# Optimization experiments

Measured on AMD Instinct MI355X. Metric: run time of the kernel, lower is better.

## Reference

```python
import jax, jax.numpy as jnp
import numpy as np

N = 50000        # nodes
E = 1600000      # edges (before self loops)
IN = 128         # in_channels
HID = 32         # hidden_channels
HEADS = 4
OUT = 16         # out_channels
B = 512          # graphs in batch
NEG_SLOPE = 0.2  # PyG GATConv default


def _uniform(key, shape, fan_in):
    s = 1.0 / np.sqrt(fan_in)
    return jax.random.uniform(key, shape, jnp.float32, -s, s)


def setup_inputs() -> dict:
    key = jax.random.key(0)
    ks = jax.random.split(key, 12)
    x = jax.random.normal(ks[0], (N, IN), jnp.float32)
    edge_index = jax.random.randint(ks[1], (2, E), 0, N, dtype=jnp.int64)
    batch = jnp.sort(jax.random.randint(ks[2], (N,), 0, B, dtype=jnp.int64))
    return {
        "x": x,
        "edge_index": edge_index,
        "batch": batch,
        "W1": _uniform(ks[3], (IN, HEADS * HID), IN),
        "att_src": _uniform(ks[4], (HEADS, HID), HID),
        "att_dst": _uniform(ks[5], (HEADS, HID), HID),
        "b1": jnp.zeros((HEADS * HID,), jnp.float32),
        "lin1_w": _uniform(ks[6], (HEADS * HID, HID), HEADS * HID),
        "lin1_b": _uniform(ks[7], (HID,), HEADS * HID),
        "lin2_w": _uniform(ks[8], (HID, OUT), HID),
        "lin2_b": _uniform(ks[9], (OUT,), HID),
    }


def _gat_conv(x, src, dst, W1, att_src, att_dst, b1):
    # h: [N, H, C]
    h = (x @ W1).reshape(N, HEADS, HID)
    a_s = (h * att_src).sum(-1)   # [N, H]
    a_d = (h * att_dst).sum(-1)   # [N, H]
    # per-edge attention logits [E', H]
    alpha = jax.nn.leaky_relu(a_s[src] + a_d[dst], negative_slope=NEG_SLOPE)
    # segment softmax over incoming edges of each destination node
    amax = jax.lax.stop_gradient(jax.ops.segment_max(alpha, dst, num_segments=N))
    ex = jnp.exp(alpha - amax[dst])
    den = jax.ops.segment_sum(ex, dst, num_segments=N)
    a = ex / (den[dst] + 1e-16)
    # weighted scatter-aggregate of source features: [N, H, C]
    out = jax.ops.segment_sum(h[src] * a[:, :, None], dst, num_segments=N)
    return out.reshape(N, HEADS * HID) + b1


def reference(x, edge_index, batch, W1, att_src, att_dst, b1, lin1_w, lin1_b, lin2_w, lin2_b):
    # add self loops (PyG GATConv default add_self_loops=True)
    loop = jnp.arange(N, dtype=edge_index.dtype)
    src = jnp.concatenate([edge_index[0], loop])
    dst = jnp.concatenate([edge_index[1], loop])
    # dropout layers are identity in eval mode
    xh = jax.nn.elu(_gat_conv(x, src, dst, W1, att_src, att_dst, b1))
    g = jax.ops.segment_sum(xh, batch, num_segments=B)  # global_add_pool -> [B, H*C]
    g = g @ lin1_w + lin1_b
    return g @ lin2_w + lin2_b
```

## Files before the change

### kernel.cpp

```cpp
#include <hip/hip_runtime.h>
#include <hip/hip_bf16.h>
#include <hip/hip_fp16.h>

#define N_NODES 50000
#define E_EDGES 1600000
#define IN_CH 128
#define HID 32
#define HEADS 4
#define HC (HEADS * HID)
#define OUT_CH 16
#define B_GRAPHS 512
#define NEG_SLOPE 0.2f
#define CAP 96
#define NB 256
#define BNODES 196
#define PCAP 7168
#define ACHUNK 4096
#define APART 391
#define ROWS_PB 64
#define GEMM_BLOCKS 782

__device__ __forceinline__ unsigned short f2bf(float f) {
    unsigned int u = __float_as_uint(f);
    unsigned int r = (u + 0x7FFFu + ((u >> 16) & 1u)) >> 16;
    return (unsigned short)r;
}

__device__ __forceinline__ float lrelu_exp(float v) {
    v = v > 0.f ? v : NEG_SLOPE * v;
    return __expf(v);
}

__global__ __launch_bounds__(256) void k_fused(const float* __restrict__ x,
                                               const float* __restrict__ W1,
                                               const float* __restrict__ att_src,
                                               const float* __restrict__ att_dst,
                                               const int* __restrict__ ei,
                                               unsigned short* __restrict__ hb,
                                               float* __restrict__ a_s,
                                               float* __restrict__ a_d,
                                               int* __restrict__ gcur,
                                               unsigned int* __restrict__ ebuf,
                                               float* __restrict__ g) {
    __shared__ float smem[12288];
    const int t = threadIdx.x;

    if (blockIdx.x < APART) {
        int* scnt = (int*)smem;
        int* sbase = scnt + NB;
        const int e0 = blockIdx.x * ACHUNK;
        int e1 = e0 + ACHUNK; if (e1 > E_EDGES) e1 = E_EDGES;
        for (int i = t; i < NB; i += 256) scnt[i] = 0;
        __syncthreads();
        const int* __restrict__ dstp = ei + E_EDGES;
        for (int e = e0 + t; e < e1; e += 256) {
            int d = dstp[e];
            atomicAdd(&scnt[d / BNODES], 1);
        }
        __syncthreads();
        for (int b = t; b < NB; b += 256) {
            sbase[b] = atomicAdd(&gcur[b], scnt[b]);
            scnt[b] = 0;
        }
        __syncthreads();
        for (int e = e0 + t; e < e1; e += 256) {
            int d = dstp[e];
            int s = ei[e];
            int b = d / BNODES;
            int dl = d - b * BNODES;
            int pos = sbase[b] + atomicAdd(&scnt[b], 1);
            if (pos < PCAP)
                ebuf[(size_t)b * PCAP + pos] = ((unsigned int)dl << 16) | (unsigned int)s;
        }
        return;
    }

    float* sX = smem;
    float* sW = smem + 8192;
    const int bid = blockIdx.x - APART;
    const int n0 = bid * ROWS_PB;

    int gt = bid * 256 + t;
    if (gt < B_GRAPHS * HC) g[gt] = 0.f;

    for (int i = t; i < ROWS_PB * 32; i += 256) {
        int r = i >> 5, c4 = i & 31;
        int n = n0 + r;
        float4 v = (n < N_NODES) ? ((const float4*)x)[(size_t)n * 32 + c4]
                                 : make_float4(0.f, 0.f, 0.f, 0.f);
        ((float4*)sX)[i] = v;
    }

    float acc[8][4];
#pragma unroll
    for (int j = 0; j < 8; j++)
#pragma unroll
        for (int c = 0; c < 4; c++) acc[j][c] = 0.f;

    const int tx = t & 31;
    const int ty = t >> 5;

    for (int kb = 0; kb < 4; kb++) {
        __syncthreads();
        for (int i = t; i < 32 * 32; i += 256) {
            ((float4*)sW)[i] =
                ((const float4*)W1)[(size_t)(kb * 32 + (i >> 5)) * 32 + (i & 31)];
        }
        __syncthreads();
#pragma unroll
        for (int kk = 0; kk < 32; kk += 4) {
            float4 w0 = *(float4*)&sW[(kk + 0) * 128 + tx * 4];
            float4 w1 = *(float4*)&sW[(kk + 1) * 128 + tx * 4];
            float4 w2 = *(float4*)&sW[(kk + 2) * 128 + tx * 4];
            float4 w3 = *(float4*)&sW[(kk + 3) * 128 + tx * 4];
#pragma unroll
            for (int j = 0; j < 8; j++) {
                float4 xv = *(float4*)&sX[(ty * 8 + j) * 128 + kb * 32 + kk];
                acc[j][0] += xv.x * w0.x + xv.y * w1.x + xv.z * w2.x + xv.w * w3.x;
                acc[j][1] += xv.x * w0.y + xv.y * w1.y + xv.z * w2.y + xv.w * w3.y;
                acc[j][2] += xv.x * w0.z + xv.y * w1.z + xv.z * w2.z + xv.w * w3.z;
                acc[j][3] += xv.x * w0.w + xv.y * w1.w + xv.z * w2.w + xv.w * w3.w;
            }
        }
    }

#pragma unroll
    for (int j = 0; j < 8; j++) {
        int n = n0 + ty * 8 + j;
        if (n < N_NODES) {
            ushort4 o;
            o.x = f2bf(acc[j][0]); o.y = f2bf(acc[j][1]);
            o.z = f2bf(acc[j][2]); o.w = f2bf(acc[j][3]);
            *(ushort4*)&hb[(size_t)n * HC + tx * 4] = o;
        }
    }

    __syncthreads();
    float* sH = smem;
#pragma unroll
    for (int j = 0; j < 8; j++) {
        float* row = &sH[(ty * 8 + j) * 129 + tx * 4];
        row[0] = acc[j][0]; row[1] = acc[j][1];
        row[2] = acc[j][2]; row[3] = acc[j][3];
    }
    __syncthreads();
    if (t < 128) {
        int r = t & 63;
        int n = n0 + r;
        const float* __restrict__ av = (t < 64) ? att_src : att_dst;
        float s0 = 0.f, s1 = 0.f, s2 = 0.f, s3 = 0.f;
#pragma unroll 4
        for (int j = 0; j < 32; j++) {
            const float* row = &sH[r * 129 + j];
            s0 += row[0]  * av[j];
            s1 += row[32] * av[32 + j];
            s2 += row[64] * av[64 + j];
            s3 += row[96] * av[96 + j];
        }
        if (n < N_NODES) {
            float* dst = (t < 64) ? a_s : a_d;
            *(float4*)(dst + (size_t)n * 4) = make_float4(s0, s1, s2, s3);
        }
    }
}

__global__ __launch_bounds__(256) void k_partB(const unsigned int* __restrict__ ebuf,
                                               const int* __restrict__ gcur,
                                               unsigned short* __restrict__ csr,
                                               int* __restrict__ cnt) {
    __shared__ unsigned short sbuf[BNODES * CAP];
    __shared__ int scnt[BNODES];
    const int t = threadIdx.x;
    const int b = blockIdx.x;
    const int dbase = b * BNODES;
    for (int i = t; i < BNODES; i += 256) {
        int d = dbase + i;
        scnt[i] = (d < N_NODES) ? 1 : 0;
        sbuf[i * CAP] = (unsigned short)d;
    }
    __syncthreads();
    int m = gcur[b]; if (m > PCAP) m = PCAP;
    for (int i = t; i < m; i += 256) {
        unsigned int p = ebuf[(size_t)b * PCAP + i];
        int dl = p >> 16;
        int s = p & 0xFFFFu;
        int c = atomicAdd(&scnt[dl], 1);
        if (c < CAP) sbuf[dl * CAP + c] = (unsigned short)s;
    }
    __syncthreads();
    const uint4* sb4 = (const uint4*)sbuf;
    uint4* g4 = (uint4*)(csr + (size_t)dbase * CAP);
    for (int i = t; i < (BNODES * CAP * 2) / 16; i += 256) g4[i] = sb4[i];
    for (int i = t; i < BNODES; i += 256) cnt[dbase + i] = scnt[i];
}

#define ANW 4
__global__ __launch_bounds__(256) void k_agg_pool(const int* __restrict__ cnt,
                                                  const unsigned short* __restrict__ csr,
                                                  const float* __restrict__ a_s,
                                                  const float* __restrict__ a_d,
                                                  const unsigned short* __restrict__ hb,
                                                  const float* __restrict__ b1,
                                                  const int* __restrict__ batch,
                                                  float* __restrict__ g) {
    __shared__ int   sS[4][CAP];
    __shared__ float sWt[4][4][100];
    const int t = threadIdx.x;
    const int wv = t >> 6;
    const int l = t & 63;
    const int head = l >> 4;
    const int c0 = 2 * l;
    const int n0 = blockIdx.x * (4 * ANW) + wv * ANW;
    const float2 bias = *(const float2*)(b1 + c0);
    float pool0 = 0.f, pool1 = 0.f;
    int cur = batch[n0];
    for (int n = n0; n < n0 + ANW; n++) {
        int b = batch[n];
        if (b != cur) {
            atomicAdd(&g[(size_t)cur * HC + c0], pool0);
            atomicAdd(&g[(size_t)cur * HC + c0 + 1], pool1);
            pool0 = pool1 = 0.f;
            cur = b;
        }
        int c = cnt[n]; if (c > CAP) c = CAP;
        float4 ad = *(const float4*)(a_d + (size_t)n * 4);
        for (int i = l; i < c; i += 64) {
            int s = csr[(size_t)n * CAP + i];
            sS[wv][i] = s;
            float4 as = *(const float4*)(a_s + (size_t)s * 4);
            sWt[wv][0][i] = lrelu_exp(as.x + ad.x);
            sWt[wv][1][i] = lrelu_exp(as.y + ad.y);
            sWt[wv][2][i] = lrelu_exp(as.z + ad.z);
            sWt[wv][3][i] = lrelu_exp(as.w + ad.w);
        }
        __asm__ volatile("" ::: "memory");
        const float* __restrict__ wrow = &sWt[wv][head][0];
        const int* __restrict__ srow = &sS[wv][0];
        float acc0 = 0.f, acc1 = 0.f, dsum = 0.f;
        int i = 0;
        for (; i + 4 <= c; i += 4) {
            int s0 = srow[i], s1 = srow[i + 1], s2 = srow[i + 2], s3 = srow[i + 3];
            float w0 = wrow[i], w1 = wrow[i + 1], w2 = wrow[i + 2], w3 = wrow[i + 3];
            unsigned int u0 = *(const unsigned int*)(hb + (size_t)s0 * HC + c0);
            unsigned int u1 = *(const unsigned int*)(hb + (size_t)s1 * HC + c0);
            unsigned int u2 = *(const unsigned int*)(hb + (size_t)s2 * HC + c0);
            unsigned int u3 = *(const unsigned int*)(hb + (size_t)s3 * HC + c0);
            dsum += (w0 + w1) + (w2 + w3);
            acc0 += w0 * __uint_as_float(u0 << 16) + w1 * __uint_as_float(u1 << 16)
                  + w2 * __uint_as_float(u2 << 16) + w3 * __uint_as_float(u3 << 16);
            acc1 += w0 * __uint_as_float(u0 & 0xFFFF0000u)
                  + w1 * __uint_as_float(u1 & 0xFFFF0000u)
                  + w2 * __uint_as_float(u2 & 0xFFFF0000u)
                  + w3 * __uint_as_float(u3 & 0xFFFF0000u);
        }
        for (; i < c; i++) {
            int s0 = srow[i];
            float w0 = wrow[i];
            unsigned int u0 = *(const unsigned int*)(hb + (size_t)s0 * HC + c0);
            dsum += w0;
            acc0 += w0 * __uint_as_float(u0 << 16);
            acc1 += w0 * __uint_as_float(u0 & 0xFFFF0000u);
        }
        __asm__ volatile("" ::: "memory");
        float inv = 1.f / (dsum + 1e-16f);
        float v0 = acc0 * inv + bias.x; v0 = v0 > 0.f ? v0 : (__expf(v0) - 1.f);
        float v1 = acc1 * inv + bias.y; v1 = v1 > 0.f ? v1 : (__expf(v1) - 1.f);
        pool0 += v0;
        pool1 += v1;
    }
    atomicAdd(&g[(size_t)cur * HC + c0], pool0);
    atomicAdd(&g[(size_t)cur * HC + c0 + 1], pool1);
}

__global__ __launch_bounds__(64) void k_mlp(const float* __restrict__ g,
                                            const float* __restrict__ w1,
                                            const float* __restrict__ bb1,
                                            const float* __restrict__ w2,
                                            const float* __restrict__ bb2,
                                            float* __restrict__ out) {
    __shared__ float sg[HC];
    __shared__ float st[HID];
    int b = blockIdx.x;
    int t = threadIdx.x;
    sg[t]      = g[(size_t)b * HC + t];
    sg[t + 64] = g[(size_t)b * HC + 64 + t];
    __syncthreads();
    if (t < HID) {
        float acc = bb1[t];
#pragma unroll 8
        for (int k = 0; k < HC; k++) acc += sg[k] * w1[(size_t)k * HID + t];
        st[t] = acc;
    }
    __syncthreads();
    if (t < OUT_CH) {
        float acc = bb2[t];
#pragma unroll
        for (int k = 0; k < HID; k++) acc += st[k] * w2[(size_t)k * OUT_CH + t];
        out[(size_t)b * OUT_CH + t] = acc;
    }
}

extern "C" void kernel_launch(void* const* d_in, const int* in_sizes, int n_in,
                              void* d_out, int out_size, void* d_ws, size_t ws_size,
                              hipStream_t stream) {
    const float* x       = (const float*)d_in[0];
    const int*   ei      = (const int*)d_in[1];
    const int*   batch   = (const int*)d_in[2];
    const float* W1      = (const float*)d_in[3];
    const float* att_src = (const float*)d_in[4];
    const float* att_dst = (const float*)d_in[5];
    const float* b1      = (const float*)d_in[6];
    const float* lin1_w  = (const float*)d_in[7];
    const float* lin1_b  = (const float*)d_in[8];
    const float* lin2_w  = (const float*)d_in[9];
    const float* lin2_b  = (const float*)d_in[10];
    float* out = (float*)d_out;

    float* ws = (float*)d_ws;
    unsigned short* hb   = (unsigned short*)ws;
    float*  a_s      = ws + 3200000;
    float*  a_d      = ws + 3400000;
    unsigned short* csr = (unsigned short*)(ws + 3600000);
    unsigned int* ebuf = (unsigned int*)(ws + 6010000);
    int*    cnt      = (int*)(ws + 7850000);
    int*    gcur     = (int*)(ws + 7901000);
    float*  g        = ws + 7902000;

    hipMemsetAsync(gcur, 0, NB * sizeof(int), stream);

    k_fused<<<APART + GEMM_BLOCKS, 256, 0, stream>>>(
        x, W1, att_src, att_dst, ei, hb, a_s, a_d, gcur, ebuf, g);
    k_partB<<<NB, 256, 0, stream>>>(ebuf, gcur, csr, cnt);
    k_agg_pool<<<N_NODES / (4 * ANW), 256, 0, stream>>>(
        cnt, csr, a_s, a_d, hb, b1, batch, g);
    k_mlp<<<B_GRAPHS, 64, 0, stream>>>(g, lin1_w, lin1_b, lin2_w, lin2_b, out);
}
```

Before: 228.6 us.

## Fuse CSR bucket build into aggregation kernel and privatize partition counters per wave

The per-bucket CSR build and the attention aggregation plus pooling now run in one kernel with 1024-thread blocks. Each wave aggregates 13 destination nodes directly from the shared-memory adjacency, so the CSR and count arrays no longer go through global memory and one launch is removed. The partition pass keeps per-wave shared counters, which spreads out shared-atomic contention. The cost is only 256 blocks of 1024 threads for the aggregation stage, which gives lower parallelism and fewer nodes in flight than the earlier 3125-block launch.

```diff
diff --git a/kernel.cpp b/kernel.cpp
--- a/kernel.cpp
+++ b/kernel.cpp
@@ -47,20 +47,28 @@
 
     if (blockIdx.x < APART) {
         int* scnt = (int*)smem;
-        int* sbase = scnt + NB;
+        int* sbase = scnt + 4 * NB;
+        const int wv = t >> 6;
         const int e0 = blockIdx.x * ACHUNK;
         int e1 = e0 + ACHUNK; if (e1 > E_EDGES) e1 = E_EDGES;
-        for (int i = t; i < NB; i += 256) scnt[i] = 0;
+        for (int i = t; i < 4 * NB; i += 256) scnt[i] = 0;
         __syncthreads();
         const int* __restrict__ dstp = ei + E_EDGES;
         for (int e = e0 + t; e < e1; e += 256) {
             int d = dstp[e];
-            atomicAdd(&scnt[d / BNODES], 1);
-        }
-        __syncthreads();
-        for (int b = t; b < NB; b += 256) {
-            sbase[b] = atomicAdd(&gcur[b], scnt[b]);
-            scnt[b] = 0;
+            atomicAdd(&scnt[wv * NB + d / BNODES], 1);
+        }
+        __syncthreads();
+        if (t < NB) {
+            int c0 = scnt[0 * NB + t], c1 = scnt[1 * NB + t];
+            int c2 = scnt[2 * NB + t], c3 = scnt[3 * NB + t];
+            int base = atomicAdd(&gcur[t], c0 + c1 + c2 + c3);
+            sbase[0 * NB + t] = base;
+            sbase[1 * NB + t] = base + c0;
+            sbase[2 * NB + t] = base + c0 + c1;
+            sbase[3 * NB + t] = base + c0 + c1 + c2;
+            scnt[0 * NB + t] = 0; scnt[1 * NB + t] = 0;
+            scnt[2 * NB + t] = 0; scnt[3 * NB + t] = 0;
         }
         __syncthreads();
         for (int e = e0 + t; e < e1; e += 256) {
@@ -68,7 +76,7 @@
             int s = ei[e];
             int b = d / BNODES;
             int dl = d - b * BNODES;
-            int pos = sbase[b] + atomicAdd(&scnt[b], 1);
+            int pos = sbase[wv * NB + b] + atomicAdd(&scnt[wv * NB + b], 1);
             if (pos < PCAP)
                 ebuf[(size_t)b * PCAP + pos] = ((unsigned int)dl << 16) | (unsigned int)s;
         }
@@ -164,23 +172,30 @@
     }
 }
 
-__global__ __launch_bounds__(256) void k_partB(const unsigned int* __restrict__ ebuf,
+#define NPW 13
+__global__ __launch_bounds__(1024) void k_aggB(const unsigned int* __restrict__ ebuf,
                                                const int* __restrict__ gcur,
-                                               unsigned short* __restrict__ csr,
-                                               int* __restrict__ cnt) {
+                                               const float* __restrict__ a_s,
+                                               const float* __restrict__ a_d,
+                                               const unsigned short* __restrict__ hb,
+                                               const float* __restrict__ b1,
+                                               const int* __restrict__ batch,
+                                               float* __restrict__ g) {
     __shared__ unsigned short sbuf[BNODES * CAP];
     __shared__ int scnt[BNODES];
+    __shared__ float sWt[16][4][97];
     const int t = threadIdx.x;
     const int b = blockIdx.x;
     const int dbase = b * BNODES;
-    for (int i = t; i < BNODES; i += 256) {
+
+    for (int i = t; i < BNODES; i += 1024) {
         int d = dbase + i;
         scnt[i] = (d < N_NODES) ? 1 : 0;
         sbuf[i * CAP] = (unsigned short)d;
     }
     __syncthreads();
     int m = gcur[b]; if (m > PCAP) m = PCAP;
-    for (int i = t; i < m; i += 256) {
+    for (int i = t; i < m; i += 1024) {
         unsigned int p = ebuf[(size_t)b * PCAP + i];
         int dl = p >> 16;
         int s = p & 0xFFFFu;
@@ -188,45 +203,33 @@
         if (c < CAP) sbuf[dl * CAP + c] = (unsigned short)s;
     }
     __syncthreads();
-    const uint4* sb4 = (const uint4*)sbuf;
-    uint4* g4 = (uint4*)(csr + (size_t)dbase * CAP);
-    for (int i = t; i < (BNODES * CAP * 2) / 16; i += 256) g4[i] = sb4[i];
-    for (int i = t; i < BNODES; i += 256) cnt[dbase + i] = scnt[i];
-}
-
-#define ANW 4
-__global__ __launch_bounds__(256) void k_agg_pool(const int* __restrict__ cnt,
-                                                  const unsigned short* __restrict__ csr,
-                                                  const float* __restrict__ a_s,
-                                                  const float* __restrict__ a_d,
-                                                  const unsigned short* __restrict__ hb,
-                                                  const float* __restrict__ b1,
-                                                  const int* __restrict__ batch,
-                                                  float* __restrict__ g) {
-    __shared__ int   sS[4][CAP];
-    __shared__ float sWt[4][4][100];
-    const int t = threadIdx.x;
+
     const int wv = t >> 6;
     const int l = t & 63;
     const int head = l >> 4;
     const int c0 = 2 * l;
-    const int n0 = blockIdx.x * (4 * ANW) + wv * ANW;
+    int nl0 = wv * NPW;
+    int nl1 = nl0 + NPW; if (nl1 > BNODES) nl1 = BNODES;
+    int gn0 = dbase + nl0;
+    if (gn0 >= N_NODES) return;
+    int gn1 = dbase + nl1; if (gn1 > N_NODES) gn1 = N_NODES;
     const float2 bias = *(const float2*)(b1 + c0);
     float pool0 = 0.f, pool1 = 0.f;
-    int cur = batch[n0];
-    for (int n = n0; n < n0 + ANW; n++) {
-        int b = batch[n];
-        if (b != cur) {
+    int cur = batch[gn0];
+    for (int n = gn0; n < gn1; n++) {
+        int bb = batch[n];
+        if (bb != cur) {
             atomicAdd(&g[(size_t)cur * HC + c0], pool0);
             atomicAdd(&g[(size_t)cur * HC + c0 + 1], pool1);
             pool0 = pool1 = 0.f;
-            cur = b;
-        }
-        int c = cnt[n]; if (c > CAP) c = CAP;
+            cur = bb;
+        }
+        int nl = n - dbase;
+        int c = scnt[nl]; if (c > CAP) c = CAP;
         float4 ad = *(const float4*)(a_d + (size_t)n * 4);
+        const unsigned short* __restrict__ srow = &sbuf[nl * CAP];
         for (int i = l; i < c; i += 64) {
-            int s = csr[(size_t)n * CAP + i];
-            sS[wv][i] = s;
+            int s = srow[i];
             float4 as = *(const float4*)(a_s + (size_t)s * 4);
             sWt[wv][0][i] = lrelu_exp(as.x + ad.x);
             sWt[wv][1][i] = lrelu_exp(as.y + ad.y);
@@ -235,7 +238,6 @@
         }
         __asm__ volatile("" ::: "memory");
         const float* __restrict__ wrow = &sWt[wv][head][0];
-        const int* __restrict__ srow = &sS[wv][0];
         float acc0 = 0.f, acc1 = 0.f, dsum = 0.f;
         int i = 0;
         for (; i + 4 <= c; i += 4) {
@@ -320,18 +322,14 @@
     unsigned short* hb   = (unsigned short*)ws;
     float*  a_s      = ws + 3200000;
     float*  a_d      = ws + 3400000;
-    unsigned short* csr = (unsigned short*)(ws + 3600000);
-    unsigned int* ebuf = (unsigned int*)(ws + 6010000);
-    int*    cnt      = (int*)(ws + 7850000);
-    int*    gcur     = (int*)(ws + 7901000);
-    float*  g        = ws + 7902000;
+    unsigned int* ebuf = (unsigned int*)(ws + 3600000);
+    int*    gcur     = (int*)(ws + 5435008);
+    float*  g        = ws + 5436000;
 
     hipMemsetAsync(gcur, 0, NB * sizeof(int), stream);
 
     k_fused<<<APART + GEMM_BLOCKS, 256, 0, stream>>>(
         x, W1, att_src, att_dst, ei, hb, a_s, a_d, gcur, ebuf, g);
-    k_partB<<<NB, 256, 0, stream>>>(ebuf, gcur, csr, cnt);
-    k_agg_pool<<<N_NODES / (4 * ANW), 256, 0, stream>>>(
-        cnt, csr, a_s, a_d, hb, b1, batch, g);
+    k_aggB<<<NB, 1024, 0, stream>>>(ebuf, gcur, a_s, a_d, hb, b1, batch, g);
     k_mlp<<<B_GRAPHS, 64, 0, stream>>>(g, lin1_w, lin1_b, lin2_w, lin2_b, out);
 }
```

Measured after the change: 228.0 us. About the same (-0.3%).
